# Performance work log

Measured on AMD Instinct MI355X. Metric: run time of the kernel, lower is better.

## Reference

```python
import jax, jax.numpy as jnp
import numpy as np

TEMPERATURE = 1.0
STRIDE = 1
PADDING = 2
RF = 5  # receptive_field_size
TREE_DEPTH = 3

# Each of the 16 binary difflogic ops op_g(a,b) is multilinear:
# op_g = c0 + c1*a + c2*b + c3*a*b. Rows ordered per the standard difflogic table:
# 0:0, 1:a&b, 2:a&~b, 3:a, 4:~a&b, 5:b, 6:xor, 7:or, 8:nor, 9:xnor,
# 10:~b, 11:a|~b, 12:~a, 13:~a|b, 14:nand, 15:1
_C = jnp.asarray(np.array([
    [0, 0, 0, 0],
    [0, 0, 0, 1],
    [0, 1, 0, -1],
    [0, 1, 0, 0],
    [0, 0, 1, -1],
    [0, 0, 1, 0],
    [0, 1, 1, -2],
    [0, 1, 1, -1],
    [1, -1, -1, 1],
    [1, -1, -1, 2],
    [1, 0, -1, 0],
    [1, 0, -1, 1],
    [1, -1, 0, 0],
    [1, -1, 0, 1],
    [1, 0, 0, -1],
    [1, 0, 0, 0]], dtype=np.float32))


def _gate(a, b, logits):
    """Soft LUT gate. a,b: (B,K,N,P); logits: (N,K,16) -> (B,K,N,P)."""
    w = jax.nn.softmax(logits / TEMPERATURE, axis=-1)          # (N,K,16)
    coef = jnp.einsum('nkg,gc->knc', w, _C)                    # (K,N,4)
    c = coef[None, :, :, None, :]                              # (1,K,N,1,4)
    return c[..., 0] + c[..., 1] * a + c[..., 2] * b + c[..., 3] * (a * b)


def setup_inputs() -> dict:
    key = jax.random.key(0)
    ks = jax.random.split(key, 8)
    B, Cin, H, W = 16, 32, 64, 64
    K, N = 64, 2 ** TREE_DEPTH  # num_kernels, leaf gates per tree
    x = jax.random.uniform(ks[0], (B, Cin, H, W), dtype=jnp.float32)
    idx_h = jax.random.randint(ks[1], (2, K, N), 0, RF, dtype=jnp.int32)
    idx_w = jax.random.randint(ks[2], (2, K, N), 0, RF, dtype=jnp.int32)
    idx_c = jax.random.randint(ks[3], (2, K, N), 0, Cin, dtype=jnp.int32)
    w0 = jax.random.normal(ks[4], (8, K, 16), dtype=jnp.float32)
    w1 = jax.random.normal(ks[5], (4, K, 16), dtype=jnp.float32)
    w2 = jax.random.normal(ks[6], (2, K, 16), dtype=jnp.float32)
    w3 = jax.random.normal(ks[7], (1, K, 16), dtype=jnp.float32)
    return {"x": x, "idx_h": idx_h, "idx_w": idx_w, "idx_c": idx_c,
            "w0": w0, "w1": w1, "w2": w2, "w3": w3}


def reference(x, idx_h, idx_w, idx_c, w0, w1, w2, w3):
    B, Cin, H, W = x.shape
    xp = jnp.pad(x, ((0, 0), (0, 0), (PADDING, PADDING), (PADDING, PADDING)))
    out_h = (H + 2 * PADDING - RF) // STRIDE + 1
    out_w = (W + 2 * PADDING - RF) // STRIDE + 1
    # Absolute gather coords per (rank-slot, kernel, leaf-gate, out_y, out_x)
    abs_h = idx_h[..., None, None] + (jnp.arange(out_h) * STRIDE)[:, None]   # (2,K,N,oh,1)
    abs_w = idx_w[..., None, None] + (jnp.arange(out_w) * STRIDE)[None, :]   # (2,K,N,1,ow)
    cc = idx_c[..., None, None]                                              # (2,K,N,1,1)
    g = xp[:, cc, abs_h, abs_w]                                # (B,2,K,N,oh,ow)
    K, N = g.shape[2], g.shape[3]
    g = g.reshape(B, 2, K, N, out_h * out_w)                   # (B,2,K,N,P)
    cur = _gate(g[:, 0], g[:, 1], w0)                          # (B,K,8,P) leaf level
    for wl in (w1, w2, w3):                                    # reduce tree: 8->4->2->1
        cur = _gate(cur[:, :, 0::2, :], cur[:, :, 1::2, :], wl)
    return cur.reshape(B, K, out_h, out_w)
```

## Files before the change

### kernel.cpp

```cpp
#include <hip/hip_runtime.h>
#include <hip/hip_bf16.h>

#define CIN 32
#define HW 64
#define KK 64
#define NLEAF 8
#define PADDING 2
#define TR 8
#define TC 16
#define WR 12
#define WC 20
#define WPOS (CIN * WR * WC)

typedef float f32x2 __attribute__((ext_vector_type(2)));

__device__ __constant__ float d_C[16][4] = {
    {0, 0, 0, 0},  {0, 0, 0, 1},  {0, 1, 0, -1}, {0, 1, 0, 0},
    {0, 0, 1, -1}, {0, 0, 1, 0},  {0, 1, 1, -2}, {0, 1, 1, -1},
    {1, -1, -1, 1},{1, -1, -1, 2},{1, 0, -1, 0}, {1, 0, -1, 1},
    {1, -1, 0, 0}, {1, -1, 0, 1}, {1, 0, 0, -1}, {1, 0, 0, 0}
};

__global__ __launch_bounds__(256) void prep_kernel(
    const int* __restrict__ idx_h, const int* __restrict__ idx_w, const int* __restrict__ idx_c,
    const float* __restrict__ w0, const float* __restrict__ w1,
    const float* __restrict__ w2, const float* __restrict__ w3,
    float* __restrict__ coefA, int* __restrict__ loffA)
{
    if (blockIdx.x == 4) {
        int k = threadIdx.x;
        if (k < KK) {
            #pragma unroll
            for (int n = 0; n < 16; ++n) {
                int s = n >> 3, leaf = n & 7;
                int o = s * (KK * NLEAF) + k * NLEAF + leaf;
                loffA[k * 16 + n] = idx_c[o] * (WR * WC) + idx_h[o] * WC + idx_w[o];
            }
        }
        return;
    }
    int t = blockIdx.x * blockDim.x + threadIdx.x;
    if (t >= KK * 15) return;
    int k = t / 15, node = t % 15;
    const float* wp; int n;
    if (node < 8)       { wp = w0; n = node; }
    else if (node < 12) { wp = w1; n = node - 8; }
    else if (node < 14) { wp = w2; n = node - 12; }
    else                { wp = w3; n = 0; }
    const float* l = wp + (n * KK + k) * 16;
    float m = l[0];
    #pragma unroll
    for (int g = 1; g < 16; ++g) m = fmaxf(m, l[g]);
    float p[16], s = 0.f;
    #pragma unroll
    for (int g = 0; g < 16; ++g) { p[g] = expf(l[g] - m); s += p[g]; }
    float inv = 1.f / s;
    float c0 = 0, c1 = 0, c2 = 0, c3 = 0;
    #pragma unroll
    for (int g = 0; g < 16; ++g) {
        float w = p[g] * inv;
        c0 = fmaf(w, d_C[g][0], c0);
        c1 = fmaf(w, d_C[g][1], c1);
        c2 = fmaf(w, d_C[g][2], c2);
        c3 = fmaf(w, d_C[g][3], c3);
    }
    float* o = coefA + (k * 60 + node * 4);
    o[0] = c0; o[1] = c1; o[2] = c2; o[3] = c3;
}

__device__ __forceinline__ f32x2 bc(float s) { return (f32x2){s, s}; }
__device__ __forceinline__ f32x2 gate2(const float* c, f32x2 a, f32x2 b) {
    return __builtin_elementwise_fma(b,
               __builtin_elementwise_fma(a, bc(c[3]), bc(c[2])),
               __builtin_elementwise_fma(a, bc(c[1]), bc(c[0])));
}

__global__ __launch_bounds__(512, 4) void logic_conv_kernel(
    const float* __restrict__ x, const int* __restrict__ loffA,
    const float* __restrict__ coefA, float* __restrict__ out)
{
    __shared__ f32x2 xt[WPOS];

    int tid = threadIdx.x;
    int bp  = blockIdx.x & 7;
    int rem = blockIdx.x >> 3;
    int t   = rem & 31;
    int kg  = rem >> 5;
    int r0  = (t >> 2) * TR;
    int c0  = (t & 3) * TC;

    const float* xb0 = x + (size_t)(2 * bp) * (CIN * HW * HW);
    const float* xb1 = xb0 + (CIN * HW * HW);

    #pragma unroll
    for (int i = 0; i < 15; ++i) {
        int e  = tid + i * 512;
        int c  = e / (WR * WC);
        int r  = e - c * (WR * WC);
        int rr = r / WC;
        int cc = r - rr * WC;
        int ih = r0 + rr - PADDING, iw = c0 + cc - PADDING;
        f32x2 v = {0.f, 0.f};
        if ((unsigned)ih < HW && (unsigned)iw < HW) {
            int go = (c * HW + ih) * HW + iw;
            v.x = xb0[go];
            v.y = xb1[go];
        }
        xt[e] = v;
    }
    __syncthreads();

    int lane = tid & 63, wave = tid >> 6;
    int tr = lane >> 4, tc = lane & 15;
    int pxe   = tr * WC + tc;
    int pxout = (r0 + tr) * HW + (c0 + tc);
    float* outB0 = out + ((size_t)(2 * bp) << 18);
    float* outB1 = outB0 + (1 << 18);

    int kbase = __builtin_amdgcn_readfirstlane(kg * 16 + wave * 2);

    #pragma unroll
    for (int p = 0; p < 2; ++p) {
        int k = kbase + p;
        const int*   L = loffA + (k << 4);
        const float* C = coefA + k * 60;

        #pragma unroll
        for (int it = 0; it < 2; ++it) {
            f32x2 g[16];
            #pragma unroll
            for (int n = 0; n < 16; ++n)
                g[n] = xt[L[n] + pxe + it * (4 * WC)];

            f32x2 v[8];
            #pragma unroll
            for (int n = 0; n < 8; ++n)
                v[n] = gate2(C + 4 * n, g[n], g[8 + n]);
            f32x2 u[4];
            #pragma unroll
            for (int n = 0; n < 4; ++n)
                u[n] = gate2(C + 32 + 4 * n, v[2 * n], v[2 * n + 1]);
            f32x2 t0 = gate2(C + 48, u[0], u[1]);
            f32x2 t1 = gate2(C + 52, u[2], u[3]);
            f32x2 r  = gate2(C + 56, t0, t1);

            int ko = (k << 12) + pxout + it * (4 * HW);
            __builtin_nontemporal_store(r.x, &outB0[ko]);
            __builtin_nontemporal_store(r.y, &outB1[ko]);
        }
    }
}

extern "C" void kernel_launch(void* const* d_in, const int* in_sizes, int n_in,
                              void* d_out, int out_size, void* d_ws, size_t ws_size,
                              hipStream_t stream) {
    const float* x     = (const float*)d_in[0];
    const int*   idx_h = (const int*)d_in[1];
    const int*   idx_w = (const int*)d_in[2];
    const int*   idx_c = (const int*)d_in[3];
    const float* w0    = (const float*)d_in[4];
    const float* w1    = (const float*)d_in[5];
    const float* w2    = (const float*)d_in[6];
    const float* w3    = (const float*)d_in[7];
    float* out   = (float*)d_out;

    float* coefA = (float*)d_ws;
    int*   loffA = (int*)((char*)d_ws + 16384);

    hipLaunchKernelGGL(prep_kernel, dim3(5), dim3(256), 0, stream,
                       idx_h, idx_w, idx_c, w0, w1, w2, w3, coefA, loffA);
    hipLaunchKernelGGL(logic_conv_kernel, dim3(1024), dim3(512), 0, stream,
                       x, loffA, coefA, out);
}
```

Before: 25.03 us.

## Process four kernels per wave and halve grid to reuse staged tiles

Each block now computes 32 output kernels instead of 16, so the grid halves and each staged shared-memory input tile is reused across twice as many kernels. The inner loop processes both row halves of a kernel together, sharing offset and coefficient loads. This reduces redundant global loads of input windows, but it lowers the block count per CU and raises register pressure, which may reduce latency hiding.

```diff
diff --git a/kernel.cpp b/kernel.cpp
--- a/kernel.cpp
+++ b/kernel.cpp
@@ -117,37 +117,46 @@
     float* outB0 = out + ((size_t)(2 * bp) << 18);
     float* outB1 = outB0 + (1 << 18);
 
-    int kbase = __builtin_amdgcn_readfirstlane(kg * 16 + wave * 2);
+    int kbase = __builtin_amdgcn_readfirstlane(kg * 32 + wave * 4);
 
-    #pragma unroll
-    for (int p = 0; p < 2; ++p) {
-        int k = kbase + p;
+    #pragma unroll 2
+    for (int i = 0; i < 4; ++i) {
+        int k = kbase + i;
         const int*   L = loffA + (k << 4);
         const float* C = coefA + k * 60;
 
+        f32x2 g0[16], g1[16];
         #pragma unroll
-        for (int it = 0; it < 2; ++it) {
-            f32x2 g[16];
-            #pragma unroll
-            for (int n = 0; n < 16; ++n)
-                g[n] = xt[L[n] + pxe + it * (4 * WC)];
+        for (int n = 0; n < 16; ++n) {
+            const f32x2* p = &xt[L[n] + pxe];
+            g0[n] = p[0];
+            g1[n] = p[80];
+        }
 
-            f32x2 v[8];
-            #pragma unroll
-            for (int n = 0; n < 8; ++n)
-                v[n] = gate2(C + 4 * n, g[n], g[8 + n]);
-            f32x2 u[4];
-            #pragma unroll
-            for (int n = 0; n < 4; ++n)
-                u[n] = gate2(C + 32 + 4 * n, v[2 * n], v[2 * n + 1]);
-            f32x2 t0 = gate2(C + 48, u[0], u[1]);
-            f32x2 t1 = gate2(C + 52, u[2], u[3]);
-            f32x2 r  = gate2(C + 56, t0, t1);
+        f32x2 v0[8], v1[8];
+        #pragma unroll
+        for (int n = 0; n < 8; ++n) {
+            v0[n] = gate2(C + 4 * n, g0[n], g0[8 + n]);
+            v1[n] = gate2(C + 4 * n, g1[n], g1[8 + n]);
+        }
+        f32x2 u0[4], u1[4];
+        #pragma unroll
+        for (int n = 0; n < 4; ++n) {
+            u0[n] = gate2(C + 32 + 4 * n, v0[2 * n], v0[2 * n + 1]);
+            u1[n] = gate2(C + 32 + 4 * n, v1[2 * n], v1[2 * n + 1]);
+        }
+        f32x2 s00 = gate2(C + 48, u0[0], u0[1]);
+        f32x2 s01 = gate2(C + 52, u0[2], u0[3]);
+        f32x2 s10 = gate2(C + 48, u1[0], u1[1]);
+        f32x2 s11 = gate2(C + 52, u1[2], u1[3]);
+        f32x2 q0  = gate2(C + 56, s00, s01);
+        f32x2 q1  = gate2(C + 56, s10, s11);
 
-            int ko = (k << 12) + pxout + it * (4 * HW);
-            __builtin_nontemporal_store(r.x, &outB0[ko]);
-            __builtin_nontemporal_store(r.y, &outB1[ko]);
-        }
+        int ko = (k << 12) + pxout;
+        __builtin_nontemporal_store(q0.x, &outB0[ko]);
+        __builtin_nontemporal_store(q0.y, &outB1[ko]);
+        __builtin_nontemporal_store(q1.x, &outB0[ko + 4 * HW]);
+        __builtin_nontemporal_store(q1.y, &outB1[ko + 4 * HW]);
     }
 }
 
@@ -169,6 +178,6 @@
 
     hipLaunchKernelGGL(prep_kernel, dim3(5), dim3(256), 0, stream,
                        idx_h, idx_w, idx_c, w0, w1, w2, w3, coefA, loffA);
-    hipLaunchKernelGGL(logic_conv_kernel, dim3(1024), dim3(512), 0, stream,
+    hipLaunchKernelGGL(logic_conv_kernel, dim3(512), dim3(512), 0, stream,
                        x, loffA, coefA, out);
 }
```

Measured after the change: 24.16 us. 1.04x faster.
